# Optimization experiments

Measured on AMD Instinct MI355X. Metric: run time of the kernel, lower is better.

## Reference

```python
import jax, jax.numpy as jnp
import numpy as np

C = 192   # channels (class attr)
N = 196   # tokens per stream; 2N = 392, R feat dim = 784
B = 256

def _pw(x, w, b):
    # 1x1 Conv1d == pointwise channel mix: x [B,Ci,L] -> [B,Co,L]
    return jnp.einsum('oi,bil->bol', w, x) + b[None, :, None]

def _bn(x, g, beta, m, v):
    # eval-mode BatchNorm1d
    inv = g / jnp.sqrt(v + 1e-5)
    return (x - m[None, :, None]) * inv[None, :, None] + beta[None, :, None]

def setup_inputs():
    key = jax.random.key(0)
    ks = jax.random.split(key, 24)
    s = 1.0 / np.sqrt(C)
    d = {}
    d['x'] = jax.random.normal(ks[0], (B, N, C), dtype=jnp.float32)
    d['y'] = jax.random.normal(ks[1], (B, N, C), dtype=jnp.float32)
    # linear_conv_1: Conv1d(C,C,1) + BN + ReLU
    d['w1'] = jax.random.normal(ks[2], (C, C), dtype=jnp.float32) * s
    d['b1'] = jax.random.normal(ks[3], (C,), dtype=jnp.float32) * 0.01
    d['g1'] = jnp.ones((C,), jnp.float32)
    d['be1'] = jnp.zeros((C,), jnp.float32)
    d['m1'] = jax.random.normal(ks[4], (C,), dtype=jnp.float32) * 0.1
    d['v1'] = jax.random.uniform(ks[5], (C,), dtype=jnp.float32) + 0.5
    # linear_conv_2
    d['w2'] = jax.random.normal(ks[6], (C, C), dtype=jnp.float32) * s
    d['b2'] = jax.random.normal(ks[7], (C,), dtype=jnp.float32) * 0.01
    d['g2'] = jnp.ones((C,), jnp.float32)
    d['be2'] = jnp.zeros((C,), jnp.float32)
    d['m2'] = jax.random.normal(ks[8], (C,), dtype=jnp.float32) * 0.1
    d['v2'] = jax.random.uniform(ks[9], (C,), dtype=jnp.float32) + 0.5
    # linear_conv_3: Conv1d(C,C,1)
    d['w3'] = jax.random.normal(ks[10], (C, C), dtype=jnp.float32) * s
    d['b3'] = jax.random.normal(ks[11], (C,), dtype=jnp.float32) * 0.01
    # linear_conv_4: Conv1d(784,784,1)
    d['w4'] = jax.random.normal(ks[12], (784, 784), dtype=jnp.float32) / np.sqrt(784)
    d['b4'] = jax.random.normal(ks[13], (784,), dtype=jnp.float32) * 0.01
    # linear_conv_5: Conv1d(C+784,1,1)
    d['w5'] = jax.random.normal(ks[14], (1, C + 784), dtype=jnp.float32) / np.sqrt(C + 784)
    d['b5'] = jax.random.normal(ks[15], (1,), dtype=jnp.float32) * 0.01
    return d

def reference(x, y, w1, b1, g1, be1, m1, v1, w2, b2, g2, be2, m2, v2, w3, b3, w4, b4, w5, b5):
    xp = jnp.swapaxes(x, 1, 2)  # [B,C,N]
    yp = jnp.swapaxes(y, 1, 2)
    phi_x = jax.nn.relu(_bn(_pw(xp, w1, b1), g1, be1, m1, v1))
    phi_y = jax.nn.relu(_bn(_pw(yp, w2, b2), g2, be2, m2, v2))
    cat_phi = jnp.concatenate([phi_x, phi_y], axis=2)            # [B,C,2N]
    A = jnp.einsum('bcn,bcm->bnm', cat_phi, cat_phi)             # [B,2N,2N]
    # R[b,i,:] = cat(A[b,i,:], A[b,:,i]) for i in 0..2N-1, then permute(0,2,1)
    R = jnp.concatenate([A, jnp.swapaxes(A, 1, 2)], axis=2)      # [B,2N,4N]
    R = jnp.swapaxes(R, 1, 2)                                    # [B,4N,2N] = [B,784,392]
    v = _pw(cat_phi, w3, b3)                                     # [B,C,392]
    v_ = _pw(R, w4, b4)                                          # [B,784,392]
    cat_v = jnp.concatenate([v, v_], axis=1)                     # [B,976,392]
    W = _pw(cat_v, w5, b5)                                       # [B,1,392]
    out = xp * W[:, :, :N] + yp * W[:, :, N:]                    # [B,C,N]
    return out
```

## Files before the change

kernel.cpp:

```cpp
#include <hip/hip_runtime.h>
#include <hip/hip_bf16.h>

typedef __attribute__((ext_vector_type(8))) short bf16x8;
typedef __attribute__((ext_vector_type(4))) float f32x4;

#define CDIM 192
#define NTOK 196
#define LTOT 392
#define BDIM 256
#define NBE 64

__device__ __forceinline__ ushort f2bf(float f) {
  uint u = __float_as_uint(f);
  u = (u + 0x7FFFu + ((u >> 16) & 1u)) >> 16;
  return (ushort)u;
}
__device__ __forceinline__ float bf2f(ushort h) {
  return __uint_as_float(((uint)h) << 16);
}
__device__ __forceinline__ uint pk2(float lo, float hi) {
  __hip_bfloat162 t = __float22bfloat162_rn(float2{lo, hi});
  uint r;
  __builtin_memcpy(&r, &t, 4);
  return r;
}
__device__ __forceinline__ float wave_reduce(float a) {
#pragma unroll
  for (int off = 32; off > 0; off >>= 1) a += __shfl_xor(a, off);
  return a;
}

__global__ __launch_bounds__(256) void prep_kernel(
    const float* __restrict__ w1, const float* __restrict__ b1, const float* __restrict__ g1,
    const float* __restrict__ be1, const float* __restrict__ m1, const float* __restrict__ v1,
    const float* __restrict__ w2, const float* __restrict__ b2, const float* __restrict__ g2,
    const float* __restrict__ be2, const float* __restrict__ m2, const float* __restrict__ v2,
    const float* __restrict__ w3, const float* __restrict__ b3,
    const float* __restrict__ w4, const float* __restrict__ b4,
    const float* __restrict__ w5, const float* __restrict__ b5,
    ushort* __restrict__ w1b, ushort* __restrict__ w2b,
    float* __restrict__ u3, float* __restrict__ u4, float* __restrict__ cvecs,
    float* __restrict__ Kc, float* __restrict__ s) {
  const int bid = blockIdx.x;
  const int wid = threadIdx.x >> 6, lane = threadIdx.x & 63;
  if (bid < NBE) {
    for (int i = bid * BDIM + threadIdx.x; i < 123264; i += NBE * BDIM) {
      if (i < 36864) {
        int o = i / CDIM;
        float inv = g1[o] * rsqrtf(v1[o] + 1e-5f);
        w1b[i] = f2bf(w1[i] * inv);
      } else if (i < 73728) {
        int j = i - 36864; int o = j / CDIM;
        float inv = g2[o] * rsqrtf(v2[o] + 1e-5f);
        w2b[j] = f2bf(w2[j] * inv);
      } else if (i < 74112) {
        int k = i - 73728; int h = k / CDIM, o = k % CDIM;
        const float* bb = h ? b2 : b1; const float* gg = h ? g2 : g1;
        const float* bee = h ? be2 : be1;
        const float* mm = h ? m2 : m1; const float* vv = h ? v2 : v1;
        float inv = gg[o] * rsqrtf(vv[o] + 1e-5f);
        cvecs[k] = (bb[o] - mm[o]) * inv + bee[o];
      } else {
        s[i - 74112] = 0.f;
      }
    }
  } else if (bid < NBE + 48) {
    int j = (bid - NBE) * 4 + wid;
    float a = 0.f;
    for (int c = lane; c < CDIM; c += 64) a += w5[c] * w3[c * CDIM + j];
    a = wave_reduce(a);
    if (lane == 0) u3[j] = a;
  } else if (bid < NBE + 48 + 98) {
    int j = (bid - NBE - 48) * 4 + wid;
    float a = 0.f;
    for (int o = lane; o < 784; o += 64)
      a += w5[CDIM + o] * (w4[o * 784 + j] + w4[o * 784 + j + LTOT]);
    a = wave_reduce(a);
    if (lane == 0) u4[j] = a;
  } else {
    if (wid == 0) {
      float a = 0.f;
      for (int i = lane; i < CDIM + 784; i += 64)
        a += (i < CDIM) ? w5[i] * b3[i] : w5[i] * b4[i - CDIM];
      a = wave_reduce(a);
      if (lane == 0) Kc[0] = a + b5[0];
    }
  }
}

__global__ __launch_bounds__(256) void phi_kernel(
    const float* __restrict__ x, const float* __restrict__ y,
    const ushort* __restrict__ w1b, const ushort* __restrict__ w2b,
    const float* __restrict__ cvecs, const float* __restrict__ u4,
    ushort* __restrict__ phiT, float* __restrict__ s) {
  const int bid = blockIdx.x;
  const int b = bid >> 2, h = (bid >> 1) & 1, g = bid & 1;
  const float* __restrict__ src = (h ? y : x) + (size_t)b * NTOK * CDIM;
  const ushort* __restrict__ wb = h ? w2b : w1b;
  __shared__ ushort Abuf[2][64 * CDIM];
  __shared__ float u4s[208];
  __shared__ float cs[CDIM];
  const int tid = threadIdx.x;
  for (int i = tid; i < 208; i += BDIM) u4s[i] = (i < NTOK) ? u4[h * NTOK + i] : 0.f;
  for (int i = tid; i < CDIM; i += BDIM) cs[i] = cvecs[h * CDIM + i];

  const int wid = tid >> 6, lane = tid & 63;
  const int lrow = lane & 15, kgrp = lane >> 4;
  const int cbase = wid * 48 + lrow;

  bf16x8 bfr[3][6];
#pragma unroll
  for (int ct = 0; ct < 3; ct++)
#pragma unroll
    for (int kk = 0; kk < 6; kk++)
      bfr[ct][kk] = *(const bf16x8*)(wb + (size_t)(cbase + ct * 16) * CDIM + kk * 32 + kgrp * 8);
  __syncthreads();
  const float csr[3] = {cs[cbase], cs[cbase + 16], cs[cbase + 32]};

  const float4* src4 = (const float4*)src;
  const int NF4 = NTOK * CDIM / 4;
  float sp[3] = {0.f, 0.f, 0.f};

  const int r0 = g * 2, r1 = r0 + 2;
  float4 pf[12];
#pragma unroll
  for (int p = 0; p < 12; p++) {
    const int fi = r0 * 3072 + p * 256 + tid;
    pf[p] = (fi < NF4) ? src4[fi] : float4{0.f, 0.f, 0.f, 0.f};
  }

  for (int r = r0; r < r1; r++) {
    ushort* Ab = &Abuf[r & 1][0];
#pragma unroll
    for (int p = 0; p < 12; p++) {
      const int fi = r * 3072 + p * 256 + tid;
      const int e = fi * 4;
      const int row = e / CDIM;
      const int col = e - row * CDIM;
      const int rl = row & 63;
      uint2 wv;
      if (fi < NF4) { wv.x = pk2(pf[p].x, pf[p].y); wv.y = pk2(pf[p].z, pf[p].w); }
      else          { wv.x = 0u; wv.y = 0u; }
      uint addr = (uint)(rl * (CDIM * 2) + col * 2);
      addr ^= (uint)((rl & 7) << 4);
      *(uint2*)((char*)Ab + addr) = wv;
    }
    if (r + 1 < r1) {
#pragma unroll
      for (int p = 0; p < 12; p++) {
        const int fi = (r + 1) * 3072 + p * 256 + tid;
        pf[p] = (fi < NF4) ? src4[fi] : float4{0.f, 0.f, 0.f, 0.f};
      }
    }
    __syncthreads();
#pragma unroll
    for (int tt = 0; tt < 4; tt++) {
      const int l0 = r * 64 + tt * 16;
      if (l0 < NTOK) {
        bf16x8 afr[6];
#pragma unroll
        for (int kk = 0; kk < 6; kk++) {
          uint addr = (uint)((tt * 16 + lrow) * (CDIM * 2) + (kk * 32 + kgrp * 8) * 2);
          addr ^= (uint)((lrow & 7) << 4);
          afr[kk] = *(const bf16x8*)((const char*)Ab + addr);
        }
        f32x4 acc0 = {0.f,0.f,0.f,0.f}, acc1 = {0.f,0.f,0.f,0.f}, acc2 = {0.f,0.f,0.f,0.f};
#pragma unroll
        for (int kk = 0; kk < 6; kk++) {
          acc0 = __builtin_amdgcn_mfma_f32_16x16x32_bf16(afr[kk], bfr[0][kk], acc0, 0, 0, 0);
          acc1 = __builtin_amdgcn_mfma_f32_16x16x32_bf16(afr[kk], bfr[1][kk], acc1, 0, 0, 0);
          acc2 = __builtin_amdgcn_mfma_f32_16x16x32_bf16(afr[kk], bfr[2][kk], acc2, 0, 0, 0);
        }
        const int lbase = l0 + 4 * kgrp;
        const float4 u4v = *(const float4*)&u4s[lbase];
        ushort* pT = phiT + ((size_t)b * LTOT + h * NTOK + lbase) * CDIM + cbase;
        auto epi = [&](const f32x4& acc, int ct, float& spc) {
          const float v0 = fmaxf(acc[0] + csr[ct], 0.f);
          const float v1 = fmaxf(acc[1] + csr[ct], 0.f);
          const float v2 = fmaxf(acc[2] + csr[ct], 0.f);
          const float v3 = fmaxf(acc[3] + csr[ct], 0.f);
          const uint p01 = pk2(v0, v1), p23 = pk2(v2, v3);
          ushort* q = pT + ct * 16;
          if (lbase + 0 < NTOK) q[0 * CDIM] = (ushort)p01;
          if (lbase + 1 < NTOK) q[1 * CDIM] = (ushort)(p01 >> 16);
          if (lbase + 2 < NTOK) q[2 * CDIM] = (ushort)p23;
          if (lbase + 3 < NTOK) q[3 * CDIM] = (ushort)(p23 >> 16);
          spc += u4v.x * v0 + u4v.y * v1 + u4v.z * v2 + u4v.w * v3;
        };
        epi(acc0, 0, sp[0]); epi(acc1, 1, sp[1]); epi(acc2, 2, sp[2]);
      }
    }
  }
#pragma unroll
  for (int ct = 0; ct < 3; ct++) {
    float v = sp[ct];
    v += __shfl_xor(v, 16);
    v += __shfl_xor(v, 32);
    if (kgrp == 0) atomicAdd(&s[b * CDIM + cbase + ct * 16], v);
  }
}

__global__ __launch_bounds__(256) void wout_kernel(
    const float* __restrict__ x, const float* __restrict__ y,
    const ushort* __restrict__ phiT, const float* __restrict__ s,
    const float* __restrict__ u3, const float* __restrict__ Kc,
    float* __restrict__ out) {
  const int bid = blockIdx.x;
  const int b = bid / 7, nt = bid % 7;
  const int n0 = nt * 28;
  __shared__ float coeff[CDIM];
  __shared__ float Wl[56];
  __shared__ float tile[28][193];
  const int tid = threadIdx.x;
  for (int i = tid; i < CDIM; i += BDIM) coeff[i] = u3[i] + s[b * CDIM + i];
  __syncthreads();
  const int wv = tid >> 6, lane = tid & 63;
  const int rloc = wv * 16 + (lane >> 2), g4 = lane & 3;
  if (rloc < 56) {
    const int lg = (rloc < 28) ? (n0 + rloc) : (NTOK + n0 + rloc - 28);
    const ushort* p = phiT + ((size_t)b * LTOT + lg) * CDIM + g4 * 48;
    float acc = 0.f;
#pragma unroll
    for (int q = 0; q < 12; q++) {
      ushort4 v = *(const ushort4*)(p + q * 4);
      const float* cf = &coeff[g4 * 48 + q * 4];
      acc += cf[0] * bf2f(v.x) + cf[1] * bf2f(v.y) +
             cf[2] * bf2f(v.z) + cf[3] * bf2f(v.w);
    }
    acc += __shfl_xor(acc, 1);
    acc += __shfl_xor(acc, 2);
    if (g4 == 0) Wl[rloc] = acc + Kc[0];
  }
  __syncthreads();
  for (int i = tid; i < 28 * 48; i += BDIM) {
    const int nl = i / 48, c4 = (i % 48) * 4;
    const size_t xi = ((size_t)b * NTOK + n0 + nl) * CDIM + c4;
    const float4 xv = *(const float4*)&x[xi];
    const float4 yv = *(const float4*)&y[xi];
    const float wx = Wl[nl], wy = Wl[28 + nl];
    tile[nl][c4 + 0] = xv.x * wx + yv.x * wy;
    tile[nl][c4 + 1] = xv.y * wx + yv.y * wy;
    tile[nl][c4 + 2] = xv.z * wx + yv.z * wy;
    tile[nl][c4 + 3] = xv.w * wx + yv.w * wy;
  }
  __syncthreads();
  for (int i = tid; i < CDIM * 7; i += BDIM) {
    const int c = i / 7, nq = i % 7;
    float4 o;
    o.x = tile[nq * 4 + 0][c]; o.y = tile[nq * 4 + 1][c];
    o.z = tile[nq * 4 + 2][c]; o.w = tile[nq * 4 + 3][c];
    *(float4*)&out[((size_t)b * CDIM + c) * NTOK + n0 + nq * 4] = o;
  }
}

extern "C" void kernel_launch(void* const* d_in, const int* in_sizes, int n_in,
                              void* d_out, int out_size, void* d_ws, size_t ws_size,
                              hipStream_t stream) {
  const float* x   = (const float*)d_in[0];
  const float* y   = (const float*)d_in[1];
  const float* w1  = (const float*)d_in[2];
  const float* b1  = (const float*)d_in[3];
  const float* g1  = (const float*)d_in[4];
  const float* be1 = (const float*)d_in[5];
  const float* m1  = (const float*)d_in[6];
  const float* v1  = (const float*)d_in[7];
  const float* w2  = (const float*)d_in[8];
  const float* b2  = (const float*)d_in[9];
  const float* g2  = (const float*)d_in[10];
  const float* be2 = (const float*)d_in[11];
  const float* m2  = (const float*)d_in[12];
  const float* v2  = (const float*)d_in[13];
  const float* w3  = (const float*)d_in[14];
  const float* b3  = (const float*)d_in[15];
  const float* w4  = (const float*)d_in[16];
  const float* b4  = (const float*)d_in[17];
  const float* w5  = (const float*)d_in[18];
  const float* b5  = (const float*)d_in[19];
  float* out = (float*)d_out;

  char* ws = (char*)d_ws;
  ushort* w1b  = (ushort*)ws;
  ushort* w2b  = (ushort*)(ws + 73728);
  float* fbase = (float*)(ws + 147456);
  float* u3    = fbase;
  float* u4    = fbase + 192;
  float* cvecs = fbase + 584;
  float* Kc    = fbase + 968;
  float* s     = fbase + 976;
  ushort* phiT = (ushort*)(ws + (1 << 22));

  prep_kernel<<<211, BDIM, 0, stream>>>(w1, b1, g1, be1, m1, v1,
                                        w2, b2, g2, be2, m2, v2,
                                        w3, b3, w4, b4, w5, b5,
                                        w1b, w2b, u3, u4, cvecs, Kc, s);
  phi_kernel<<<1024, BDIM, 0, stream>>>(x, y, w1b, w2b, cvecs, u4, phiT, s);
  wout_kernel<<<256 * 7, BDIM, 0, stream>>>(x, y, phiT, s, u3, Kc, out);
}
```

Before: 68.72 us.

## Stage phi output in LDS for coalesced stores; one block per batch-stream

Each phi block now handles a whole (batch, stream) pair in 32-row chunks instead of splitting it over two blocks of 64-row chunks, halving the grid to 512 blocks. The MFMA epilogue writes bf16 results into a swizzled shared buffer, then the block copies them to global phiT with 16-byte coalesced stores instead of scattered 2-byte stores. This cuts uncoalesced global write traffic and redundant weight fragment loads per block. In exchange it adds an extra barrier per chunk and gives fewer blocks for latency hiding.

```diff
diff --git a/kernel.cpp b/kernel.cpp
--- a/kernel.cpp
+++ b/kernel.cpp
@@ -93,15 +93,15 @@
     const ushort* __restrict__ w1b, const ushort* __restrict__ w2b,
     const float* __restrict__ cvecs, const float* __restrict__ u4,
     ushort* __restrict__ phiT, float* __restrict__ s) {
-  const int bid = blockIdx.x;
-  const int b = bid >> 2, h = (bid >> 1) & 1, g = bid & 1;
+  const int bh = blockIdx.x, b = bh >> 1, h = bh & 1;
   const float* __restrict__ src = (h ? y : x) + (size_t)b * NTOK * CDIM;
   const ushort* __restrict__ wb = h ? w2b : w1b;
-  __shared__ ushort Abuf[2][64 * CDIM];
-  __shared__ float u4s[208];
+  __shared__ ushort Abuf[2][32 * CDIM];
+  __shared__ ushort Obuf[32 * CDIM];
+  __shared__ float u4s[224];
   __shared__ float cs[CDIM];
   const int tid = threadIdx.x;
-  for (int i = tid; i < 208; i += BDIM) u4s[i] = (i < NTOK) ? u4[h * NTOK + i] : 0.f;
+  for (int i = tid; i < 224; i += BDIM) u4s[i] = (i < NTOK) ? u4[h * NTOK + i] : 0.f;
   for (int i = tid; i < CDIM; i += BDIM) cs[i] = cvecs[h * CDIM + i];
 
   const int wid = tid >> 6, lane = tid & 63;
@@ -121,23 +121,20 @@
   const int NF4 = NTOK * CDIM / 4;
   float sp[3] = {0.f, 0.f, 0.f};
 
-  const int r0 = g * 2, r1 = r0 + 2;
-  float4 pf[12];
-#pragma unroll
-  for (int p = 0; p < 12; p++) {
-    const int fi = r0 * 3072 + p * 256 + tid;
-    pf[p] = (fi < NF4) ? src4[fi] : float4{0.f, 0.f, 0.f, 0.f};
-  }
-
-  for (int r = r0; r < r1; r++) {
+  float4 pf[6];
+#pragma unroll
+  for (int p = 0; p < 6; p++) {
+    pf[p] = src4[p * 256 + tid];
+  }
+
+  for (int r = 0; r < 7; r++) {
     ushort* Ab = &Abuf[r & 1][0];
 #pragma unroll
-    for (int p = 0; p < 12; p++) {
-      const int fi = r * 3072 + p * 256 + tid;
-      const int e = fi * 4;
-      const int row = e / CDIM;
-      const int col = e - row * CDIM;
-      const int rl = row & 63;
+    for (int p = 0; p < 6; p++) {
+      const int fi = r * 1536 + p * 256 + tid;
+      const int rowg = fi / 48;
+      const int col = (fi - rowg * 48) * 4;
+      const int rl = rowg & 31;
       uint2 wv;
       if (fi < NF4) { wv.x = pk2(pf[p].x, pf[p].y); wv.y = pk2(pf[p].z, pf[p].w); }
       else          { wv.x = 0u; wv.y = 0u; }
@@ -145,50 +142,61 @@
       addr ^= (uint)((rl & 7) << 4);
       *(uint2*)((char*)Ab + addr) = wv;
     }
-    if (r + 1 < r1) {
-#pragma unroll
-      for (int p = 0; p < 12; p++) {
-        const int fi = (r + 1) * 3072 + p * 256 + tid;
+    if (r < 6) {
+#pragma unroll
+      for (int p = 0; p < 6; p++) {
+        const int fi = (r + 1) * 1536 + p * 256 + tid;
         pf[p] = (fi < NF4) ? src4[fi] : float4{0.f, 0.f, 0.f, 0.f};
       }
     }
     __syncthreads();
 #pragma unroll
-    for (int tt = 0; tt < 4; tt++) {
-      const int l0 = r * 64 + tt * 16;
-      if (l0 < NTOK) {
-        bf16x8 afr[6];
-#pragma unroll
-        for (int kk = 0; kk < 6; kk++) {
-          uint addr = (uint)((tt * 16 + lrow) * (CDIM * 2) + (kk * 32 + kgrp * 8) * 2);
-          addr ^= (uint)((lrow & 7) << 4);
-          afr[kk] = *(const bf16x8*)((const char*)Ab + addr);
+    for (int tt = 0; tt < 2; tt++) {
+      bf16x8 afr[6];
+#pragma unroll
+      for (int kk = 0; kk < 6; kk++) {
+        uint addr = (uint)((tt * 16 + lrow) * (CDIM * 2) + (kk * 32 + kgrp * 8) * 2);
+        addr ^= (uint)((lrow & 7) << 4);
+        afr[kk] = *(const bf16x8*)((const char*)Ab + addr);
+      }
+      f32x4 acc0 = {0.f,0.f,0.f,0.f}, acc1 = {0.f,0.f,0.f,0.f}, acc2 = {0.f,0.f,0.f,0.f};
+#pragma unroll
+      for (int kk = 0; kk < 6; kk++) {
+        acc0 = __builtin_amdgcn_mfma_f32_16x16x32_bf16(afr[kk], bfr[0][kk], acc0, 0, 0, 0);
+        acc1 = __builtin_amdgcn_mfma_f32_16x16x32_bf16(afr[kk], bfr[1][kk], acc1, 0, 0, 0);
+        acc2 = __builtin_amdgcn_mfma_f32_16x16x32_bf16(afr[kk], bfr[2][kk], acc2, 0, 0, 0);
+      }
+      const int ll = tt * 16 + 4 * kgrp;
+      const float4 u4v = *(const float4*)&u4s[r * 32 + ll];
+      auto epi = [&](const f32x4& acc, int ct, float& spc) {
+        const float v0 = fmaxf(acc[0] + csr[ct], 0.f);
+        const float v1 = fmaxf(acc[1] + csr[ct], 0.f);
+        const float v2 = fmaxf(acc[2] + csr[ct], 0.f);
+        const float v3 = fmaxf(acc[3] + csr[ct], 0.f);
+        const uint p01 = pk2(v0, v1), p23 = pk2(v2, v3);
+        const int c = cbase + ct * 16;
+#pragma unroll
+        for (int j = 0; j < 4; j++) {
+          const int row = ll + j;
+          uint addr = (uint)(row * (CDIM * 2) + c * 2);
+          addr ^= (uint)((row & 7) << 4);
+          const uint piece = (j == 0) ? (p01 & 0xFFFFu) : (j == 1) ? (p01 >> 16)
+                           : (j == 2) ? (p23 & 0xFFFFu) : (p23 >> 16);
+          *(ushort*)((char*)Obuf + addr) = (ushort)piece;
         }
-        f32x4 acc0 = {0.f,0.f,0.f,0.f}, acc1 = {0.f,0.f,0.f,0.f}, acc2 = {0.f,0.f,0.f,0.f};
-#pragma unroll
-        for (int kk = 0; kk < 6; kk++) {
-          acc0 = __builtin_amdgcn_mfma_f32_16x16x32_bf16(afr[kk], bfr[0][kk], acc0, 0, 0, 0);
-          acc1 = __builtin_amdgcn_mfma_f32_16x16x32_bf16(afr[kk], bfr[1][kk], acc1, 0, 0, 0);
-          acc2 = __builtin_amdgcn_mfma_f32_16x16x32_bf16(afr[kk], bfr[2][kk], acc2, 0, 0, 0);
-        }
-        const int lbase = l0 + 4 * kgrp;
-        const float4 u4v = *(const float4*)&u4s[lbase];
-        ushort* pT = phiT + ((size_t)b * LTOT + h * NTOK + lbase) * CDIM + cbase;
-        auto epi = [&](const f32x4& acc, int ct, float& spc) {
-          const float v0 = fmaxf(acc[0] + csr[ct], 0.f);
-          const float v1 = fmaxf(acc[1] + csr[ct], 0.f);
-          const float v2 = fmaxf(acc[2] + csr[ct], 0.f);
-          const float v3 = fmaxf(acc[3] + csr[ct], 0.f);
-          const uint p01 = pk2(v0, v1), p23 = pk2(v2, v3);
-          ushort* q = pT + ct * 16;
-          if (lbase + 0 < NTOK) q[0 * CDIM] = (ushort)p01;
-          if (lbase + 1 < NTOK) q[1 * CDIM] = (ushort)(p01 >> 16);
-          if (lbase + 2 < NTOK) q[2 * CDIM] = (ushort)p23;
-          if (lbase + 3 < NTOK) q[3 * CDIM] = (ushort)(p23 >> 16);
-          spc += u4v.x * v0 + u4v.y * v1 + u4v.z * v2 + u4v.w * v3;
-        };
-        epi(acc0, 0, sp[0]); epi(acc1, 1, sp[1]); epi(acc2, 2, sp[2]);
-      }
+        spc += u4v.x * v0 + u4v.y * v1 + u4v.z * v2 + u4v.w * v3;
+      };
+      epi(acc0, 0, sp[0]); epi(acc1, 1, sp[1]); epi(acc2, 2, sp[2]);
+    }
+    __syncthreads();
+    const int rows = min(32, NTOK - r * 32);
+    const int nel = rows * CDIM;
+    ushort* dst = phiT + ((size_t)b * LTOT + h * NTOK + r * 32) * CDIM;
+    for (int off = tid * 8; off < nel; off += BDIM * 8) {
+      const int row = off / CDIM;
+      uint addr = (uint)(off * 2) ^ (uint)((row & 7) << 4);
+      uint4 v = *(const uint4*)((const char*)Obuf + addr);
+      *(uint4*)(dst + off) = v;
     }
   }
 #pragma unroll
@@ -293,6 +301,6 @@
                                         w2, b2, g2, be2, m2, v2,
                                         w3, b3, w4, b4, w5, b5,
                                         w1b, w2b, u3, u4, cvecs, Kc, s);
-  phi_kernel<<<1024, BDIM, 0, stream>>>(x, y, w1b, w2b, cvecs, u4, phiT, s);
+  phi_kernel<<<512, BDIM, 0, stream>>>(x, y, w1b, w2b, cvecs, u4, phiT, s);
   wout_kernel<<<256 * 7, BDIM, 0, stream>>>(x, y, phiT, s, u3, Kc, out);
 }
```

New measurement: 62.16 us. 1.11x faster.
